# Optimization experiments

Measured on AMD Instinct MI355X. Metric: run time of the kernel, lower is better.

Reference implementation:

```python
import jax, jax.numpy as jnp
import numpy as np

NX, NQ, NU, NY = 256, 64, 8, 4
N = 65536
EPS = 0.01
STD = 0.5


def setup_inputs() -> dict:
    key = jax.random.key(0)
    ks = jax.random.split(key, 8)
    return {
        "x": jax.random.normal(ks[0], (N, NX), jnp.float32),
        "u": jax.random.normal(ks[1], (N, NU), jnp.float32),
        "X": jax.random.normal(ks[2], (NX + NQ, NX + NQ), jnp.float32) * STD,
        "U": jax.random.normal(ks[3], (NX, NQ), jnp.float32) * STD,
        "Y1": jax.random.normal(ks[4], (NX, NX), jnp.float32) * STD,
        "XP": jax.random.normal(ks[5], (NX, NX), jnp.float32) * STD,
        "B2": jax.random.normal(ks[6], (NX, NU), jnp.float32) * STD,
        "D12": jax.random.normal(ks[7], (NQ, NU), jnp.float32) * STD,
        "bv": jnp.zeros((NQ,), jnp.float32),
        "t": 0,
    }


def _constrained(X, U, Y1, XP):
    # updateParameters(): build A, B1, C1, D11 from unconstrained params.
    P = XP @ XP.T + EPS * jnp.eye(NX, dtype=XP.dtype)
    H = X @ X.T + EPS * jnp.eye(NX + NQ, dtype=X.dtype)
    H11, H12, H22 = H[:NX, :NX], H[:NX, NX:], H[NX:, NX:]
    Y = -0.5 * (H11 + Y1 - Y1.T)
    Pinv = jnp.linalg.inv(P)
    A = Pinv @ Y                                   # [nx, nx]
    lam = 0.5 * jnp.diagonal(H22)                  # Lambda diagonal
    D11 = -jnp.tril(H22, -1) / lam[:, None]        # strictly lower triangular [nq, nq]
    C1 = U.T / lam[:, None]                        # [nq, nx]
    B1 = Pinv @ (-H12 - U)                         # [nx, nq]
    return A, B1, C1, D11


def _calc_w(base, D11):
    # Forward substitution: w_i = relu(base_i + sum_{j<i} D11[i,j] * w_j).
    # D11 is strictly lower triangular and unfilled w columns are zero, so a
    # full matvec against the carry is exact.
    nq = base.shape[1]

    def step(w, inp):
        i, row, b_col = inp                        # row: [nq], b_col: [Nbatch]
        wi = jax.nn.relu(b_col + w @ row)
        return w.at[:, i].set(wi), None

    w0 = jnp.zeros_like(base)
    w, _ = jax.lax.scan(step, w0, (jnp.arange(nq), D11, base.T))
    return w


def reference(x, u, X, U, Y1, XP, B2, D12, bv, t):
    A, B1, C1, D11 = _constrained(X, U, Y1, XP)
    base = x @ C1.T + u @ D12.T + bv               # [N, nq]
    w = _calc_w(base, D11)
    x_dot = x @ A.T + w @ B1.T + u @ B2.T          # [N, nx]
    return x_dot
```

## Files before the change

### kernel.cpp

```cpp
#include <hip/hip_runtime.h>

#define EPS_C 0.01f

typedef __attribute__((ext_vector_type(8))) short short8;
typedef __attribute__((ext_vector_type(4))) float f32x4;
typedef __attribute__((ext_vector_type(4))) unsigned short u16x4;
typedef __attribute__((ext_vector_type(8))) unsigned short u16x8;

#define WS_H    0
#define WS_C    102400
#define WS_C2   167936
#define WS_Y    233472
#define WS_RHS  299008
#define WS_D11  331776
#define WS_WFH  419840
#define WS_WFM  464896
#define WS_WFL  509952
#define WS_BBH  555008
#define WS_BBM  564224
#define WS_BBL  573440
#define WS_WG   582656
#define WS_E0   4776960
#define WS_E1   4781056

__device__ __forceinline__ int wfoff(int n, int k) {
    return (((n >> 4) * 44 + (k >> 5) * 4 + ((k >> 3) & 3)) << 7) + ((n & 15) << 3) + (k & 7);
}
__device__ __forceinline__ int bboff(int n, int k) {
    return (((n >> 4) * 36 + (k >> 5) * 4 + ((k >> 3) & 3)) << 7) + ((n & 15) << 3) + (k & 7);
}

__device__ __forceinline__ unsigned short f2bf(float f) {
    unsigned int u = __float_as_uint(f);
    unsigned int r = (u + 0x7fffu + ((u >> 16) & 1u)) >> 16;
    return (unsigned short)r;
}
__device__ __forceinline__ float bf2f(unsigned short h) {
    return __uint_as_float(((unsigned int)h) << 16);
}
__device__ __forceinline__ void split1(float f, unsigned short& h, unsigned short& m, unsigned short& l) {
    h = f2bf(f);
    float r1 = f - bf2f(h);
    m = f2bf(r1);
    l = f2bf(r1 - bf2f(m));
}
__device__ __forceinline__ void split8(const float* v, short8& h8, short8& m8, short8& l8) {
#pragma unroll
    for (int j = 0; j < 8; ++j) {
        unsigned short h, m, l;
        split1(v[j], h, m, l);
        h8[j] = (short)h; m8[j] = (short)m; l8[j] = (short)l;
    }
}

__global__ void k_build(const float* __restrict__ Xm, const float* __restrict__ XPm,
                        float* __restrict__ H, float* __restrict__ P) {
    int idx = blockIdx.x * 256 + threadIdx.x;
    if (idx < 102400) {
        int i = idx / 320, j = idx - i * 320;
        const float4* a = (const float4*)(Xm + i * 320);
        const float4* b = (const float4*)(Xm + j * 320);
        float s = 0.f;
        for (int k = 0; k < 80; ++k) {
            float4 va = a[k], vb = b[k];
            s += va.x * vb.x + va.y * vb.y + va.z * vb.z + va.w * vb.w;
        }
        H[idx] = (i == j) ? s + EPS_C : s;
    } else {
        idx -= 102400;
        if (idx < 65536) {
            int i = idx >> 8, j = idx & 255;
            const float4* a = (const float4*)(XPm + i * 256);
            const float4* b = (const float4*)(XPm + j * 256);
            float s = 0.f;
            for (int k = 0; k < 64; ++k) {
                float4 va = a[k], vb = b[k];
                s += va.x * vb.x + va.y * vb.y + va.z * vb.z + va.w * vb.w;
            }
            P[idx] = (i == j) ? s + EPS_C : s;
        }
    }
}

__global__ void __launch_bounds__(256) k_derived(const float* __restrict__ H, const float* __restrict__ Um,
                          const float* __restrict__ Y1, const float* __restrict__ B2,
                          const float* __restrict__ D12,
                          float* __restrict__ Y, float* __restrict__ RHS,
                          float* __restrict__ D11g,
                          unsigned short* __restrict__ Bh, unsigned short* __restrict__ Bm,
                          unsigned short* __restrict__ Bl,
                          unsigned short* __restrict__ Bbh, unsigned short* __restrict__ Bbm,
                          unsigned short* __restrict__ Bbl,
                          const float* __restrict__ C0, float* __restrict__ E0) {
    __shared__ __align__(16) float M[64 * 68];
    __shared__ __align__(16) float Rs[8 * 68];
    __shared__ __align__(16) float Ts[64 * 8];
    __shared__ float E8s[8 * 9];
    const int tid = threadIdx.x;
    if (blockIdx.x == 441) {
        const int ti = tid & 15, tj = tid >> 4;
#pragma unroll
        for (int t = 0; t < 4; ++t) {
            int e = tid + t * 256;
            int r = e >> 4, c4 = e & 15;
            float4 v = *(const float4*)&C0[(size_t)r * 256 + c4 * 4];
            *(float4*)&M[r * 68 + c4 * 4] = v;
        }
        __syncthreads();
        for (int s = 0; s < 8; ++s) {
            if (tid < 64) {
                const int lane = tid;
                float e8[8];
#pragma unroll
                for (int j = 0; j < 8; ++j) e8[j] = 0.f;
                if (lane < 8) {
#pragma unroll
                    for (int j = 0; j < 8; ++j) e8[j] = M[(s * 8 + lane) * 68 + s * 8 + j];
                }
#pragma unroll
                for (int k = 0; k < 8; ++k) {
                    const float p = __shfl(e8[k], k);
                    const float rinv = 1.0f / p;
                    const float f = -e8[k] * rinv;
                    const bool isk = (lane == k);
#pragma unroll
                    for (int j = 0; j < 8; ++j) {
                        const float prj = __shfl(e8[j], k);
                        if (j == k) e8[j] = isk ? rinv : f;
                        else        e8[j] = isk ? prj * rinv : fmaf(f, prj, e8[j]);
                    }
                }
                if (lane < 8) {
#pragma unroll
                    for (int j = 0; j < 8; ++j) E8s[lane * 9 + j] = e8[j];
                }
            }
            __syncthreads();
#pragma unroll
            for (int t = 0; t < 2; ++t) {
                int e = tid + t * 256;
                int r = e >> 6, c = e & 63;
                Rs[r * 68 + c] = M[(s * 8 + r) * 68 + c];
            }
#pragma unroll
            for (int t = 0; t < 2; ++t) {
                int e = tid + t * 256;
                int i = e >> 3, c = e & 7;
                float acc = 0.f;
#pragma unroll
                for (int j = 0; j < 8; ++j) acc = fmaf(M[i * 68 + s * 8 + j], E8s[j * 9 + c], acc);
                Ts[i * 8 + c] = acc;
            }
            __syncthreads();
            {
                const bool rowIn = ((ti >> 1) == s);
                const bool colIn = ((tj >> 1) == s);
                const int i0 = ti * 4, j0 = tj * 4;
                float nv[4][4];
                if (rowIn && colIn) {
#pragma unroll
                    for (int r = 0; r < 4; ++r)
#pragma unroll
                        for (int d = 0; d < 4; ++d)
                            nv[r][d] = E8s[(i0 - s * 8 + r) * 9 + (j0 - s * 8 + d)];
                } else if (rowIn) {
#pragma unroll
                    for (int r = 0; r < 4; ++r)
#pragma unroll
                        for (int d = 0; d < 4; ++d) {
                            float acc = 0.f;
#pragma unroll
                            for (int c = 0; c < 8; ++c)
                                acc = fmaf(E8s[(i0 - s * 8 + r) * 9 + c], Rs[c * 68 + j0 + d], acc);
                            nv[r][d] = acc;
                        }
                } else if (colIn) {
#pragma unroll
                    for (int r = 0; r < 4; ++r)
#pragma unroll
                        for (int d = 0; d < 4; ++d)
                            nv[r][d] = -Ts[(i0 + r) * 8 + (j0 - s * 8 + d)];
                } else {
#pragma unroll
                    for (int r = 0; r < 4; ++r)
#pragma unroll
                        for (int d = 0; d < 4; ++d) {
                            float acc = M[(i0 + r) * 68 + j0 + d];
#pragma unroll
                            for (int c = 0; c < 8; ++c)
                                acc = fmaf(-Ts[(i0 + r) * 8 + c], Rs[c * 68 + j0 + d], acc);
                            nv[r][d] = acc;
                        }
                }
#pragma unroll
                for (int r = 0; r < 4; ++r)
#pragma unroll
                    for (int d = 0; d < 4; ++d) M[(i0 + r) * 68 + j0 + d] = nv[r][d];
            }
            __syncthreads();
        }
#pragma unroll
        for (int t = 0; t < 4; ++t) {
            int e = tid + t * 256;
            int r = e >> 4, c4 = e & 15;
            float4 v = *(const float4*)&M[r * 68 + c4 * 4];
            *(float4*)&E0[(size_t)r * 64 + c4 * 4] = v;
        }
        return;
    }
    int idx = blockIdx.x * 256 + tid;
    if (idx < 65536) {
        int i = idx >> 8, j = idx & 255;
        Y[idx] = -0.5f * (H[i * 320 + j] + Y1[i * 256 + j] - Y1[j * 256 + i]);
        return;
    }
    idx -= 65536;
    if (idx < 16384) {
        RHS[idx] = -H[(idx >> 6) * 320 + 256 + (idx & 63)] - Um[idx];
        return;
    }
    idx -= 16384;
    if (idx < 4096) {
        int q = idx >> 6, j = idx & 63;
        float lam = 0.5f * H[(256 + q) * 320 + 256 + q];
        D11g[idx] = (j < q) ? -H[(256 + q) * 320 + 256 + j] / lam : 0.f;
        return;
    }
    idx -= 4096;
    if (idx < 8192) {
        int o = idx >> 5, cc = idx & 31;
        float f = (cc < 8) ? B2[o * 8 + cc] : 0.f;
        unsigned short h, m, l;
        split1(f, h, m, l);
        int off = wfoff(o, 256 + cc);
        Bh[off] = h; Bm[off] = m; Bl[off] = l;
        return;
    }
    idx -= 8192;
    if (idx < 18432) {
        int q = idx / 288, k = idx - q * 288;
        float f;
        if (k < 256) {
            float lam = 0.5f * H[(256 + q) * 320 + 256 + q];
            f = Um[(size_t)k * 64 + q] / lam;
        } else if (k < 264) f = D12[(size_t)q * 8 + (k - 256)];
        else f = 0.f;
        unsigned short h, m, l;
        split1(f, h, m, l);
        int off = bboff(q, k);
        Bbh[off] = h; Bbm[off] = m; Bbl[off] = l;
    }
}

__global__ void __launch_bounds__(256) k_gjS(const float* __restrict__ Cold, float* __restrict__ Cnew,
                                             const float* __restrict__ E, float* __restrict__ Eout,
                                             int b, int nb) {
    const int I = blockIdx.x >> 2, J = blockIdx.x & 3;
    const int tid = threadIdx.x;
    const int ti = tid & 15, tj = tid >> 4;
    if (I == b && J == b) {
        const int r = tid >> 2, seg = tid & 3;
#pragma unroll
        for (int t = 0; t < 4; ++t) {
            float4 v = *(const float4*)&E[(size_t)r * 64 + seg * 16 + t * 4];
            *(float4*)&Cnew[(size_t)(b * 64 + r) * 256 + b * 64 + seg * 16 + t * 4] = v;
        }
        return;
    }
    __shared__ __align__(16) float Es[64 * 68];
    __shared__ __align__(16) float S1[64 * 68];
    __shared__ __align__(16) float S2[64 * 68];
    for (int e = tid; e < 1024; e += 256) {
        int r = e >> 4, c4 = e & 15;
        float4 v = *(const float4*)&E[(size_t)r * 64 + c4 * 4];
        *(float4*)&Es[r * 68 + c4 * 4] = v;
    }
    if (I == b) {
        for (int e = tid; e < 1024; e += 256) {
            int r = e >> 4, c4 = e & 15;
            float4 v = *(const float4*)&Cold[(size_t)(b * 64 + r) * 256 + J * 64 + c4 * 4];
            *(float4*)&S1[r * 68 + c4 * 4] = v;
        }
        __syncthreads();
        float acc[4][4];
#pragma unroll
        for (int r = 0; r < 4; ++r)
#pragma unroll
            for (int d = 0; d < 4; ++d) acc[r][d] = 0.f;
        for (int mm = 0; mm < 64; ++mm) {
            float a4[4], b4[4];
#pragma unroll
            for (int d = 0; d < 4; ++d) { a4[d] = Es[(ti * 4 + d) * 68 + mm]; b4[d] = S1[mm * 68 + tj * 4 + d]; }
#pragma unroll
            for (int r = 0; r < 4; ++r)
#pragma unroll
                for (int d = 0; d < 4; ++d) acc[r][d] = fmaf(a4[r], b4[d], acc[r][d]);
        }
#pragma unroll
        for (int r = 0; r < 4; ++r) {
            float4 v = {acc[r][0], acc[r][1], acc[r][2], acc[r][3]};
            *(float4*)&Cnew[(size_t)(b * 64 + ti * 4 + r) * 256 + J * 64 + tj * 4] = v;
        }
        return;
    }
    if (J == b) {
        for (int e = tid; e < 1024; e += 256) {
            int r = e >> 4, c4 = e & 15;
            float4 v = *(const float4*)&Cold[(size_t)(I * 64 + r) * 256 + b * 64 + c4 * 4];
            *(float4*)&S1[r * 68 + c4 * 4] = v;
        }
        __syncthreads();
        float acc[4][4];
#pragma unroll
        for (int r = 0; r < 4; ++r)
#pragma unroll
            for (int d = 0; d < 4; ++d) acc[r][d] = 0.f;
        for (int kk = 0; kk < 64; ++kk) {
            float a4[4], b4[4];
#pragma unroll
            for (int d = 0; d < 4; ++d) { a4[d] = S1[(ti * 4 + d) * 68 + kk]; b4[d] = Es[kk * 68 + tj * 4 + d]; }
#pragma unroll
            for (int r = 0; r < 4; ++r)
#pragma unroll
                for (int d = 0; d < 4; ++d) acc[r][d] = fmaf(a4[r], b4[d], acc[r][d]);
        }
#pragma unroll
        for (int r = 0; r < 4; ++r) {
            float4 v = {-acc[r][0], -acc[r][1], -acc[r][2], -acc[r][3]};
            *(float4*)&Cnew[(size_t)(I * 64 + ti * 4 + r) * 256 + b * 64 + tj * 4] = v;
        }
        return;
    }
    for (int e = tid; e < 1024; e += 256) {
        int r = e >> 4, c4 = e & 15;
        float4 v = *(const float4*)&Cold[(size_t)(I * 64 + r) * 256 + b * 64 + c4 * 4];
        *(float4*)&S1[r * 68 + c4 * 4] = v;
        float4 w = *(const float4*)&Cold[(size_t)(b * 64 + r) * 256 + J * 64 + c4 * 4];
        *(float4*)&S2[r * 68 + c4 * 4] = w;
    }
    __syncthreads();
    float t4[4][4];
#pragma unroll
    for (int r = 0; r < 4; ++r)
#pragma unroll
        for (int d = 0; d < 4; ++d) t4[r][d] = 0.f;
    for (int kk = 0; kk < 64; ++kk) {
        float a4[4], b4[4];
#pragma unroll
        for (int d = 0; d < 4; ++d) { a4[d] = S1[(ti * 4 + d) * 68 + kk]; b4[d] = Es[kk * 68 + tj * 4 + d]; }
#pragma unroll
        for (int r = 0; r < 4; ++r)
#pragma unroll
            for (int d = 0; d < 4; ++d) t4[r][d] = fmaf(a4[r], b4[d], t4[r][d]);
    }
    __syncthreads();
#pragma unroll
    for (int r = 0; r < 4; ++r)
#pragma unroll
        for (int d = 0; d < 4; ++d) S1[(ti * 4 + r) * 68 + tj * 4 + d] = t4[r][d];
    __syncthreads();
    float acc[4][4];
#pragma unroll
    for (int r = 0; r < 4; ++r) {
        float4 cv = *(const float4*)&Cold[(size_t)(I * 64 + ti * 4 + r) * 256 + J * 64 + tj * 4];
        acc[r][0] = cv.x; acc[r][1] = cv.y; acc[r][2] = cv.z; acc[r][3] = cv.w;
    }
    for (int kk = 0; kk < 64; ++kk) {
        float a4[4], b4[4];
#pragma unroll
        for (int d = 0; d < 4; ++d) { a4[d] = S1[(ti * 4 + d) * 68 + kk]; b4[d] = S2[kk * 68 + tj * 4 + d]; }
#pragma unroll
        for (int r = 0; r < 4; ++r)
#pragma unroll
            for (int d = 0; d < 4; ++d) acc[r][d] = fmaf(-a4[r], b4[d], acc[r][d]);
    }
#pragma unroll
    for (int r = 0; r < 4; ++r) {
        float4 v = {acc[r][0], acc[r][1], acc[r][2], acc[r][3]};
        *(float4*)&Cnew[(size_t)(I * 64 + ti * 4 + r) * 256 + J * 64 + tj * 4] = v;
    }
    if (I == nb && J == nb) {
        float* M   = Es;
        float* Rs2 = S2;
        float* Ts2 = S2 + 1024;
        float* E8s = S2 + 1664;
        __syncthreads();
#pragma unroll
        for (int r = 0; r < 4; ++r)
#pragma unroll
            for (int d = 0; d < 4; ++d)
                M[(ti * 4 + r) * 68 + tj * 4 + d] = acc[r][d];
        __syncthreads();
        for (int s = 0; s < 8; ++s) {
            if (tid < 64) {
                const int lane = tid;
                float e8[8];
#pragma unroll
                for (int j = 0; j < 8; ++j) e8[j] = 0.f;
                if (lane < 8) {
#pragma unroll
                    for (int j = 0; j < 8; ++j) e8[j] = M[(s * 8 + lane) * 68 + s * 8 + j];
                }
#pragma unroll
                for (int k = 0; k < 8; ++k) {
                    const float p = __shfl(e8[k], k);
                    const float rinv = 1.0f / p;
                    const float f = -e8[k] * rinv;
                    const bool isk = (lane == k);
#pragma unroll
                    for (int j = 0; j < 8; ++j) {
                        const float prj = __shfl(e8[j], k);
                        if (j == k) e8[j] = isk ? rinv : f;
                        else        e8[j] = isk ? prj * rinv : fmaf(f, prj, e8[j]);
                    }
                }
                if (lane < 8) {
#pragma unroll
                    for (int j = 0; j < 8; ++j) E8s[lane * 9 + j] = e8[j];
                }
            }
            __syncthreads();
#pragma unroll
            for (int t = 0; t < 2; ++t) {
                int e = tid + t * 256;
                int r = e >> 6, c = e & 63;
                Rs2[r * 68 + c] = M[(s * 8 + r) * 68 + c];
            }
#pragma unroll
            for (int t = 0; t < 2; ++t) {
                int e = tid + t * 256;
                int i = e >> 3, c = e & 7;
                float a2 = 0.f;
#pragma unroll
                for (int j = 0; j < 8; ++j) a2 = fmaf(M[i * 68 + s * 8 + j], E8s[j * 9 + c], a2);
                Ts2[i * 8 + c] = a2;
            }
            __syncthreads();
            {
                const bool rowIn = ((ti >> 1) == s);
                const bool colIn = ((tj >> 1) == s);
                const int i0 = ti * 4, j0 = tj * 4;
                float nv[4][4];
                if (rowIn && colIn) {
#pragma unroll
                    for (int r = 0; r < 4; ++r)
#pragma unroll
                        for (int d = 0; d < 4; ++d)
                            nv[r][d] = E8s[(i0 - s * 8 + r) * 9 + (j0 - s * 8 + d)];
                } else if (rowIn) {
#pragma unroll
                    for (int r = 0; r < 4; ++r)
#pragma unroll
                        for (int d = 0; d < 4; ++d) {
                            float a2 = 0.f;
#pragma unroll
                            for (int c = 0; c < 8; ++c)
                                a2 = fmaf(E8s[(i0 - s * 8 + r) * 9 + c], Rs2[c * 68 + j0 + d], a2);
                            nv[r][d] = a2;
                        }
                } else if (colIn) {
#pragma unroll
                    for (int r = 0; r < 4; ++r)
#pragma unroll
                        for (int d = 0; d < 4; ++d)
                            nv[r][d] = -Ts2[(i0 + r) * 8 + (j0 - s * 8 + d)];
                } else {
#pragma unroll
                    for (int r = 0; r < 4; ++r)
#pragma unroll
                        for (int d = 0; d < 4; ++d) {
                            float a2 = M[(i0 + r) * 68 + j0 + d];
#pragma unroll
                            for (int c = 0; c < 8; ++c)
                                a2 = fmaf(-Ts2[(i0 + r) * 8 + c], Rs2[c * 68 + j0 + d], a2);
                            nv[r][d] = a2;
                        }
                }
#pragma unroll
                for (int r = 0; r < 4; ++r)
#pragma unroll
                    for (int d = 0; d < 4; ++d) M[(i0 + r) * 68 + j0 + d] = nv[r][d];
            }
            __syncthreads();
        }
#pragma unroll
        for (int t = 0; t < 4; ++t) {
            int e = tid + t * 256;
            int r = e >> 4, c4 = e & 15;
            float4 v = *(const float4*)&M[r * 68 + c4 * 4];
            *(float4*)&Eout[(size_t)r * 64 + c4 * 4] = v;
        }
    }
}

__global__ void __launch_bounds__(256) k_apply2(const float* __restrict__ PI, const float* __restrict__ Y,
                                                const float* __restrict__ RHS,
                                                unsigned short* __restrict__ Bh, unsigned short* __restrict__ Bm,
                                                unsigned short* __restrict__ Bl) {
    const int i0 = ((int)blockIdx.x / 5) * 64;
    const int c0 = ((int)blockIdx.x % 5) * 64;
    __shared__ __align__(16) float S1[64 * 68], S2[64 * 68];
    const int tid = threadIdx.x;
    const int ti = tid & 15, tj = tid >> 4;
    float acc[4][4];
#pragma unroll
    for (int r = 0; r < 4; ++r)
#pragma unroll
        for (int d = 0; d < 4; ++d) acc[r][d] = 0.f;
    for (int kc = 0; kc < 4; ++kc) {
        __syncthreads();
        for (int e = tid; e < 1024; e += 256) {
            int i = e >> 4, k4 = e & 15;
            float4 v = *(const float4*)&PI[(size_t)(i0 + i) * 256 + kc * 64 + k4 * 4];
            S1[(k4 * 4 + 0) * 68 + i] = v.x;
            S1[(k4 * 4 + 1) * 68 + i] = v.y;
            S1[(k4 * 4 + 2) * 68 + i] = v.z;
            S1[(k4 * 4 + 3) * 68 + i] = v.w;
            float4 w;
            if (c0 < 256) w = *(const float4*)&Y[(size_t)(kc * 64 + i) * 256 + c0 + k4 * 4];
            else          w = *(const float4*)&RHS[(size_t)(kc * 64 + i) * 64 + k4 * 4];
            *(float4*)&S2[i * 68 + k4 * 4] = w;
        }
        __syncthreads();
        for (int kk = 0; kk < 64; ++kk) {
            float4 pv = *(const float4*)&S1[kk * 68 + ti * 4];
            float4 gv = *(const float4*)&S2[kk * 68 + tj * 4];
            float p4[4] = {pv.x, pv.y, pv.z, pv.w};
            float g4[4] = {gv.x, gv.y, gv.z, gv.w};
#pragma unroll
            for (int r = 0; r < 4; ++r)
#pragma unroll
                for (int d = 0; d < 4; ++d) acc[r][d] = fmaf(p4[r], g4[d], acc[r][d]);
        }
    }
    const int pc0 = (c0 < 256) ? c0 : 288;
#pragma unroll
    for (int r = 0; r < 4; ++r)
#pragma unroll
        for (int d = 0; d < 4; ++d) {
            unsigned short h, m, l;
            split1(acc[r][d], h, m, l);
            int off = wfoff(i0 + ti * 4 + r, pc0 + tj * 4 + d);
            Bh[off] = h; Bm[off] = m; Bl[off] = l;
        }
}

#define XSTR 264
__global__ void __launch_bounds__(256, 3) k_base(const float* __restrict__ x, const float* __restrict__ u,
                                                 const unsigned short* __restrict__ Bbh,
                                                 const unsigned short* __restrict__ Bbm,
                                                 const unsigned short* __restrict__ Bbl,
                                                 const float* __restrict__ bv,
                                                 float* __restrict__ wg) {
    __shared__ __align__(16) unsigned short Ah[32 * XSTR];
    __shared__ __align__(16) unsigned short Am[32 * XSTR];
    __shared__ __align__(16) unsigned short Al[32 * XSTR];
    const int tid = threadIdx.x;
    const int r0 = blockIdx.x * 32;
    {
        const float4* xg4 = (const float4*)(x + (size_t)r0 * 256);
#pragma unroll
        for (int i = 0; i < 8; ++i) {
            int e = tid + i * 256, r = e >> 6, c4 = e & 63;
            float4 v = xg4[e];
            float vv[4] = {v.x, v.y, v.z, v.w};
            u16x4 hv, mv, lv;
#pragma unroll
            for (int j = 0; j < 4; ++j) {
                unsigned short h, m, l;
                split1(vv[j], h, m, l);
                hv[j] = h; mv[j] = m; lv[j] = l;
            }
            *(u16x4*)&Ah[r * XSTR + c4 * 4] = hv;
            *(u16x4*)&Am[r * XSTR + c4 * 4] = mv;
            *(u16x4*)&Al[r * XSTR + c4 * 4] = lv;
        }
    }
    __syncthreads();
    const int lane = tid & 63, wid = tid >> 6;
    const int n0 = wid * 16;
    const int lr = lane & 15, lg = lane >> 4;
    const int lk = lg * 8;
    const int fb = wid * 4608 + lg * 128 + lr * 8;
    f32x4 acc[2];
    acc[0] = (f32x4){0.f, 0.f, 0.f, 0.f};
    acc[1] = (f32x4){0.f, 0.f, 0.f, 0.f};
    for (int kt = 0; kt < 9; ++kt) {
        const int ka = kt * 32 + lk;
        short8 a_h[2], a_m[2], a_l[2];
        if (kt < 8) {
            a_h[0] = *(const short8*)&Ah[lr * XSTR + ka];
            a_h[1] = *(const short8*)&Ah[(16 + lr) * XSTR + ka];
            a_m[0] = *(const short8*)&Am[lr * XSTR + ka];
            a_m[1] = *(const short8*)&Am[(16 + lr) * XSTR + ka];
            a_l[0] = *(const short8*)&Al[lr * XSTR + ka];
            a_l[1] = *(const short8*)&Al[(16 + lr) * XSTR + ka];
        } else {
            if (lg == 0) {
                float vv[8];
                const float4* up = (const float4*)&u[(size_t)(r0 + lr) * 8];
                float4 v0 = up[0], v1 = up[1];
                vv[0] = v0.x; vv[1] = v0.y; vv[2] = v0.z; vv[3] = v0.w;
                vv[4] = v1.x; vv[5] = v1.y; vv[6] = v1.z; vv[7] = v1.w;
                split8(vv, a_h[0], a_m[0], a_l[0]);
                const float4* up2 = (const float4*)&u[(size_t)(r0 + 16 + lr) * 8];
                float4 w0 = up2[0], w1 = up2[1];
                vv[0] = w0.x; vv[1] = w0.y; vv[2] = w0.z; vv[3] = w0.w;
                vv[4] = w1.x; vv[5] = w1.y; vv[6] = w1.z; vv[7] = w1.w;
                split8(vv, a_h[1], a_m[1], a_l[1]);
            } else {
                short8 z = {0, 0, 0, 0, 0, 0, 0, 0};
                a_h[0] = z; a_h[1] = z; a_m[0] = z; a_m[1] = z; a_l[0] = z; a_l[1] = z;
            }
        }
        const int off = fb + kt * 512;
        short8 b_h = *(const short8*)&Bbh[off];
        short8 b_m = *(const short8*)&Bbm[off];
        short8 b_l = *(const short8*)&Bbl[off];
#pragma unroll
        for (int m = 0; m < 2; ++m) {
            acc[m] = __builtin_amdgcn_mfma_f32_16x16x32_bf16(a_h[m], b_h, acc[m], 0, 0, 0);
            acc[m] = __builtin_amdgcn_mfma_f32_16x16x32_bf16(a_m[m], b_h, acc[m], 0, 0, 0);
            acc[m] = __builtin_amdgcn_mfma_f32_16x16x32_bf16(a_h[m], b_m, acc[m], 0, 0, 0);
            acc[m] = __builtin_amdgcn_mfma_f32_16x16x32_bf16(a_l[m], b_h, acc[m], 0, 0, 0);
            acc[m] = __builtin_amdgcn_mfma_f32_16x16x32_bf16(a_m[m], b_m, acc[m], 0, 0, 0);
            acc[m] = __builtin_amdgcn_mfma_f32_16x16x32_bf16(a_h[m], b_l, acc[m], 0, 0, 0);
        }
    }
    const float bvv = bv[n0 + lr];
#pragma unroll
    for (int m = 0; m < 2; ++m)
#pragma unroll
        for (int j = 0; j < 4; ++j)
            wg[(size_t)(r0 + m * 16 + lg * 4 + j) * 64 + n0 + lr] = acc[m][j] + bvv;
}

__global__ void __launch_bounds__(256) k_rec(float* __restrict__ wg, const float* __restrict__ D11g) {
    __shared__ float D[64 * 64];
    const int tid = threadIdx.x;
#pragma unroll
    for (int t = 0; t < 16; ++t) D[tid + t * 256] = D11g[tid + t * 256];
    __syncthreads();
    const size_t r = (size_t)blockIdx.x * 256 + tid;
    float w[64];
    float* wr = wg + r * 64;
#pragma unroll
    for (int c = 0; c < 16; ++c) {
        float4 v = *(const float4*)&wr[c * 4];
        w[4 * c] = v.x; w[4 * c + 1] = v.y; w[4 * c + 2] = v.z; w[4 * c + 3] = v.w;
    }
    w[0] = fmaxf(w[0], 0.f);
#pragma unroll
    for (int i = 1; i < 64; ++i) {
        float s0 = w[i], s1 = 0.f, s2 = 0.f, s3 = 0.f;
#pragma unroll
        for (int j = 0; j + 3 < i; j += 4) {
            s0 = fmaf(w[j + 0], D[i * 64 + j + 0], s0);
            s1 = fmaf(w[j + 1], D[i * 64 + j + 1], s1);
            s2 = fmaf(w[j + 2], D[i * 64 + j + 2], s2);
            s3 = fmaf(w[j + 3], D[i * 64 + j + 3], s3);
        }
#pragma unroll
        for (int j = i & ~3; j < i; ++j) s0 = fmaf(w[j], D[i * 64 + j], s0);
        w[i] = fmaxf((s0 + s1) + (s2 + s3), 0.f);
    }
#pragma unroll
    for (int c = 0; c < 16; ++c) {
        float4 v = {w[4 * c], w[4 * c + 1], w[4 * c + 2], w[4 * c + 3]};
        *(float4*)&wr[c * 4] = v;
    }
}

__global__ void __launch_bounds__(256, 3) k_m2(const float* __restrict__ x, const float* __restrict__ wg,
                                               const float* __restrict__ u,
                                               const unsigned short* __restrict__ Bh,
                                               const unsigned short* __restrict__ Bm,
                                               const unsigned short* __restrict__ Bl,
                                               float* __restrict__ out) {
    __shared__ __align__(16) unsigned short Ah[32 * XSTR];
    __shared__ __align__(16) unsigned short Am[32 * XSTR];
    __shared__ __align__(16) unsigned short Al[32 * XSTR];
    const int tid = threadIdx.x;
    const int r0 = blockIdx.x * 32;
    {
        const float4* xg4 = (const float4*)(x + (size_t)r0 * 256);
#pragma unroll
        for (int i = 0; i < 8; ++i) {
            int e = tid + i * 256, r = e >> 6, c4 = e & 63;
            float4 v = xg4[e];
            float vv[4] = {v.x, v.y, v.z, v.w};
            u16x4 hv, mv, lv;
#pragma unroll
            for (int j = 0; j < 4; ++j) {
                unsigned short h, m, l;
                split1(vv[j], h, m, l);
                hv[j] = h; mv[j] = m; lv[j] = l;
            }
            *(u16x4*)&Ah[r * XSTR + c4 * 4] = hv;
            *(u16x4*)&Am[r * XSTR + c4 * 4] = mv;
            *(u16x4*)&Al[r * XSTR + c4 * 4] = lv;
        }
    }
    __syncthreads();
    const int lane = tid & 63, wid = tid >> 6;
    const int n0 = wid * 64;
    const int lr = lane & 15, lg = lane >> 4;
    const int lk = lg * 8;
    const int lgoff = lg * 128 + lr * 8;
    int fb[4];
#pragma unroll
    for (int nf = 0; nf < 4; ++nf) fb[nf] = (wid * 4 + nf) * 5632 + lgoff;
    f32x4 acc[2][4];
#pragma unroll
    for (int m = 0; m < 2; ++m)
#pragma unroll
        for (int nf = 0; nf < 4; ++nf) acc[m][nf] = (f32x4){0.f, 0.f, 0.f, 0.f};

#define M2_MFMA6()                                                                               \
    for (int nf = 0; nf < 4; ++nf) {                                                             \
        for (int m = 0; m < 2; ++m) {                                                            \
            acc[m][nf] = __builtin_amdgcn_mfma_f32_16x16x32_bf16(a_h[m], b_h[nf], acc[m][nf], 0, 0, 0); \
            acc[m][nf] = __builtin_amdgcn_mfma_f32_16x16x32_bf16(a_m[m], b_h[nf], acc[m][nf], 0, 0, 0); \
// ... 55 lines not shown
    }
    for (int kt = 9; kt < 11; ++kt) {
        const int wc = (kt - 9) * 32 + lk;
        short8 a_h[2], a_m[2], a_l[2];
        {
            float vv[8];
            const float4* wp = (const float4*)&wg[(size_t)(r0 + lr) * 64 + wc];
            float4 v0 = wp[0], v1 = wp[1];
            vv[0] = v0.x; vv[1] = v0.y; vv[2] = v0.z; vv[3] = v0.w;
            vv[4] = v1.x; vv[5] = v1.y; vv[6] = v1.z; vv[7] = v1.w;
            split8(vv, a_h[0], a_m[0], a_l[0]);
            const float4* wp2 = (const float4*)&wg[(size_t)(r0 + 16 + lr) * 64 + wc];
            float4 w0 = wp2[0], w1 = wp2[1];
            vv[0] = w0.x; vv[1] = w0.y; vv[2] = w0.z; vv[3] = w0.w;
            vv[4] = w1.x; vv[5] = w1.y; vv[6] = w1.z; vv[7] = w1.w;
            split8(vv, a_h[1], a_m[1], a_l[1]);
        }
        short8 b_h[4], b_m[4], b_l[4];
#pragma unroll
        for (int nf = 0; nf < 4; ++nf) {
            const int off = fb[nf] + kt * 512;
            b_h[nf] = *(const short8*)&Bh[off];
            b_m[nf] = *(const short8*)&Bm[off];
            b_l[nf] = *(const short8*)&Bl[off];
        }
#pragma unroll
        for (int nf = 0; nf < 4; ++nf) {
#pragma unroll
            for (int m = 0; m < 2; ++m) {
                acc[m][nf] = __builtin_amdgcn_mfma_f32_16x16x32_bf16(a_h[m], b_h[nf], acc[m][nf], 0, 0, 0);
                acc[m][nf] = __builtin_amdgcn_mfma_f32_16x16x32_bf16(a_m[m], b_h[nf], acc[m][nf], 0, 0, 0);
                acc[m][nf] = __builtin_amdgcn_mfma_f32_16x16x32_bf16(a_h[m], b_m[nf], acc[m][nf], 0, 0, 0);
                acc[m][nf] = __builtin_amdgcn_mfma_f32_16x16x32_bf16(a_l[m], b_h[nf], acc[m][nf], 0, 0, 0);
                acc[m][nf] = __builtin_amdgcn_mfma_f32_16x16x32_bf16(a_m[m], b_m[nf], acc[m][nf], 0, 0, 0);
                acc[m][nf] = __builtin_amdgcn_mfma_f32_16x16x32_bf16(a_h[m], b_l[nf], acc[m][nf], 0, 0, 0);
                acc[m][nf] = __builtin_amdgcn_mfma_f32_16x16x32_bf16(a_m[m], b_l[nf], acc[m][nf], 0, 0, 0);
                acc[m][nf] = __builtin_amdgcn_mfma_f32_16x16x32_bf16(a_l[m], b_m[nf], acc[m][nf], 0, 0, 0);
            }
        }
    }
#pragma unroll
    for (int m = 0; m < 2; ++m)
#pragma unroll
        for (int nf = 0; nf < 4; ++nf)
#pragma unroll
            for (int j = 0; j < 4; ++j)
                out[(size_t)(r0 + m * 16 + lg * 4 + j) * 256 + n0 + nf * 16 + lr] = acc[m][nf][j];
}

extern "C" void kernel_launch(void* const* d_in, const int* in_sizes, int n_in,
                              void* d_out, int out_size, void* d_ws, size_t ws_size,
                              hipStream_t stream) {
    const float* x   = (const float*)d_in[0];
    const float* u   = (const float*)d_in[1];
    const float* Xm  = (const float*)d_in[2];
    const float* Um  = (const float*)d_in[3];
    const float* Y1  = (const float*)d_in[4];
    const float* XPm = (const float*)d_in[5];
    const float* B2  = (const float*)d_in[6];
    const float* D12 = (const float*)d_in[7];
    const float* bv  = (const float*)d_in[8];
    float* out = (float*)d_out;
    float* ws  = (float*)d_ws;

    float* H    = ws + WS_H;
    float* C0   = ws + WS_C;
    float* C1   = ws + WS_C2;
    float* Y    = ws + WS_Y;
    float* RHS  = ws + WS_RHS;
    float* D11g = ws + WS_D11;
    float* E0   = ws + WS_E0;
    float* E1   = ws + WS_E1;
    unsigned short* Bh  = (unsigned short*)(ws + WS_WFH);
    unsigned short* Bm  = (unsigned short*)(ws + WS_WFM);
    unsigned short* Bl  = (unsigned short*)(ws + WS_WFL);
    unsigned short* Bbh = (unsigned short*)(ws + WS_BBH);
    unsigned short* Bbm = (unsigned short*)(ws + WS_BBM);
    unsigned short* Bbl = (unsigned short*)(ws + WS_BBL);
    float* wg = ws + WS_WG;

    k_build<<<656, 256, 0, stream>>>(Xm, XPm, H, C0);
    k_derived<<<442, 256, 0, stream>>>(H, Um, Y1, B2, D12, Y, RHS, D11g,
                                       Bh, Bm, Bl, Bbh, Bbm, Bbl, C0, E0);
    k_base<<<2048, 256, 0, stream>>>(x, u, Bbh, Bbm, Bbl, bv, wg);
    k_rec<<<256, 256, 0, stream>>>(wg, D11g);
    k_gjS<<<16, 256, 0, stream>>>(C0, C1, E0, E1, 0, 1);
    k_gjS<<<16, 256, 0, stream>>>(C1, C0, E1, E0, 1, 2);
    k_gjS<<<16, 256, 0, stream>>>(C0, C1, E0, E1, 2, 3);
    k_gjS<<<16, 256, 0, stream>>>(C1, C0, E1, E0, 3, -1);
    k_apply2<<<20, 256, 0, stream>>>(C0, Y, RHS, Bh, Bm, Bl);
    k_m2<<<2048, 256, 0, stream>>>(x, wg, u, Bh, Bm, Bl, out);
}
```

Before: 338.0 us.

## Fold first two Gauss-Jordan sweeps into k_base and k_rec as extra blocks

The first two block Gauss-Jordan sweeps of the P inversion are merged into the k_base and k_rec launches as 16 extra blocks each, run on otherwise idle CUs. The intent is to remove two small serial kernel launches and overlap the inversion chain with the batch work. The sweep and 64x64 inversion code is factored into shared device functions. In exchange, k_base and k_rec now reserve a larger shared-memory array sized for the sweep, which may lower their occupancy.

```diff
diff --git a/kernel.cpp b/kernel.cpp
--- a/kernel.cpp
+++ b/kernel.cpp
@@ -78,6 +78,252 @@
                 s += va.x * vb.x + va.y * vb.y + va.z * vb.z + va.w * vb.w;
             }
             P[idx] = (i == j) ? s + EPS_C : s;
+        }
+    }
+}
+
+__device__ __forceinline__ void inv64_lds(float* M, float* Rs, float* Ts, float* E8s,
+                                          int tid, int ti, int tj) {
+    for (int s = 0; s < 8; ++s) {
+        if (tid < 64) {
+            const int lane = tid;
+            float e8[8];
+#pragma unroll
+            for (int j = 0; j < 8; ++j) e8[j] = 0.f;
+            if (lane < 8) {
+#pragma unroll
+                for (int j = 0; j < 8; ++j) e8[j] = M[(s * 8 + lane) * 68 + s * 8 + j];
+            }
+#pragma unroll
+            for (int k = 0; k < 8; ++k) {
+                const float p = __shfl(e8[k], k);
+                const float rinv = 1.0f / p;
+                const float f = -e8[k] * rinv;
+                const bool isk = (lane == k);
+#pragma unroll
+                for (int j = 0; j < 8; ++j) {
+                    const float prj = __shfl(e8[j], k);
+                    if (j == k) e8[j] = isk ? rinv : f;
+                    else        e8[j] = isk ? prj * rinv : fmaf(f, prj, e8[j]);
+                }
+            }
+            if (lane < 8) {
+#pragma unroll
+                for (int j = 0; j < 8; ++j) E8s[lane * 9 + j] = e8[j];
+            }
+        }
+        __syncthreads();
+#pragma unroll
+        for (int t = 0; t < 2; ++t) {
+            int e = tid + t * 256;
+            int r = e >> 6, c = e & 63;
+            Rs[r * 68 + c] = M[(s * 8 + r) * 68 + c];
+        }
+#pragma unroll
+        for (int t = 0; t < 2; ++t) {
+            int e = tid + t * 256;
+            int i = e >> 3, c = e & 7;
+            float acc = 0.f;
+#pragma unroll
+            for (int j = 0; j < 8; ++j) acc = fmaf(M[i * 68 + s * 8 + j], E8s[j * 9 + c], acc);
+            Ts[i * 8 + c] = acc;
+        }
+        __syncthreads();
+        {
+            const bool rowIn = ((ti >> 1) == s);
+            const bool colIn = ((tj >> 1) == s);
+            const int i0 = ti * 4, j0 = tj * 4;
+            float nv[4][4];
+            if (rowIn && colIn) {
+#pragma unroll
+                for (int r = 0; r < 4; ++r)
+#pragma unroll
+                    for (int d = 0; d < 4; ++d)
+                        nv[r][d] = E8s[(i0 - s * 8 + r) * 9 + (j0 - s * 8 + d)];
+            } else if (rowIn) {
+#pragma unroll
+                for (int r = 0; r < 4; ++r)
+#pragma unroll
+                    for (int d = 0; d < 4; ++d) {
+                        float acc = 0.f;
+#pragma unroll
+                        for (int c = 0; c < 8; ++c)
+                            acc = fmaf(E8s[(i0 - s * 8 + r) * 9 + c], Rs[c * 68 + j0 + d], acc);
+                        nv[r][d] = acc;
+                    }
+            } else if (colIn) {
+#pragma unroll
+                for (int r = 0; r < 4; ++r)
+#pragma unroll
+                    for (int d = 0; d < 4; ++d)
+                        nv[r][d] = -Ts[(i0 + r) * 8 + (j0 - s * 8 + d)];
+            } else {
+#pragma unroll
+                for (int r = 0; r < 4; ++r)
+#pragma unroll
+                    for (int d = 0; d < 4; ++d) {
+                        float acc = M[(i0 + r) * 68 + j0 + d];
+#pragma unroll
+                        for (int c = 0; c < 8; ++c)
+                            acc = fmaf(-Ts[(i0 + r) * 8 + c], Rs[c * 68 + j0 + d], acc);
+                        nv[r][d] = acc;
+                    }
+            }
+#pragma unroll
+            for (int r = 0; r < 4; ++r)
+#pragma unroll
+                for (int d = 0; d < 4; ++d) M[(i0 + r) * 68 + j0 + d] = nv[r][d];
+        }
+        __syncthreads();
+    }
+}
+
+__device__ void gj_sweep(float* SM, const float* __restrict__ Cold, float* __restrict__ Cnew,
+                         const float* __restrict__ E, float* __restrict__ Eout,
+                         int b, int nb, int bid) {
+    float* Es = SM;
+    float* S1 = SM + 4352;
+    float* S2 = SM + 8704;
+    const int tid = threadIdx.x;
+    const int I = bid >> 2, J = bid & 3;
+    const int ti = tid & 15, tj = tid >> 4;
+    if (I == b && J == b) {
+        const int r = tid >> 2, seg = tid & 3;
+#pragma unroll
+        for (int t = 0; t < 4; ++t) {
+            float4 v = *(const float4*)&E[(size_t)r * 64 + seg * 16 + t * 4];
+            *(float4*)&Cnew[(size_t)(b * 64 + r) * 256 + b * 64 + seg * 16 + t * 4] = v;
+        }
+        return;
+    }
+    for (int e = tid; e < 1024; e += 256) {
+        int r = e >> 4, c4 = e & 15;
+        float4 v = *(const float4*)&E[(size_t)r * 64 + c4 * 4];
+        *(float4*)&Es[r * 68 + c4 * 4] = v;
+    }
+    if (I == b) {
+        for (int e = tid; e < 1024; e += 256) {
+            int r = e >> 4, c4 = e & 15;
+            float4 v = *(const float4*)&Cold[(size_t)(b * 64 + r) * 256 + J * 64 + c4 * 4];
+            *(float4*)&S1[r * 68 + c4 * 4] = v;
+        }
+        __syncthreads();
+        float acc[4][4];
+#pragma unroll
+        for (int r = 0; r < 4; ++r)
+#pragma unroll
+            for (int d = 0; d < 4; ++d) acc[r][d] = 0.f;
+        for (int mm = 0; mm < 64; ++mm) {
+            float a4[4], b4[4];
+#pragma unroll
+            for (int d = 0; d < 4; ++d) { a4[d] = Es[(ti * 4 + d) * 68 + mm]; b4[d] = S1[mm * 68 + tj * 4 + d]; }
+#pragma unroll
+            for (int r = 0; r < 4; ++r)
+#pragma unroll
+                for (int d = 0; d < 4; ++d) acc[r][d] = fmaf(a4[r], b4[d], acc[r][d]);
+        }
+#pragma unroll
+        for (int r = 0; r < 4; ++r) {
+            float4 v = {acc[r][0], acc[r][1], acc[r][2], acc[r][3]};
+            *(float4*)&Cnew[(size_t)(b * 64 + ti * 4 + r) * 256 + J * 64 + tj * 4] = v;
+        }
+        return;
+    }
+    if (J == b) {
+        for (int e = tid; e < 1024; e += 256) {
+            int r = e >> 4, c4 = e & 15;
+            float4 v = *(const float4*)&Cold[(size_t)(I * 64 + r) * 256 + b * 64 + c4 * 4];
+            *(float4*)&S1[r * 68 + c4 * 4] = v;
+        }
+        __syncthreads();
+        float acc[4][4];
+#pragma unroll
+        for (int r = 0; r < 4; ++r)
+#pragma unroll
+            for (int d = 0; d < 4; ++d) acc[r][d] = 0.f;
+        for (int kk = 0; kk < 64; ++kk) {
+            float a4[4], b4[4];
+#pragma unroll
+            for (int d = 0; d < 4; ++d) { a4[d] = S1[(ti * 4 + d) * 68 + kk]; b4[d] = Es[kk * 68 + tj * 4 + d]; }
+#pragma unroll
+            for (int r = 0; r < 4; ++r)
+#pragma unroll
+                for (int d = 0; d < 4; ++d) acc[r][d] = fmaf(a4[r], b4[d], acc[r][d]);
+        }
+#pragma unroll
+        for (int r = 0; r < 4; ++r) {
+            float4 v = {-acc[r][0], -acc[r][1], -acc[r][2], -acc[r][3]};
+            *(float4*)&Cnew[(size_t)(I * 64 + ti * 4 + r) * 256 + b * 64 + tj * 4] = v;
+        }
+        return;
+    }
+    for (int e = tid; e < 1024; e += 256) {
+        int r = e >> 4, c4 = e & 15;
+        float4 v = *(const float4*)&Cold[(size_t)(I * 64 + r) * 256 + b * 64 + c4 * 4];
+        *(float4*)&S1[r * 68 + c4 * 4] = v;
+        float4 w = *(const float4*)&Cold[(size_t)(b * 64 + r) * 256 + J * 64 + c4 * 4];
+        *(float4*)&S2[r * 68 + c4 * 4] = w;
+    }
+    __syncthreads();
+    float t4[4][4];
+#pragma unroll
+    for (int r = 0; r < 4; ++r)
+#pragma unroll
+        for (int d = 0; d < 4; ++d) t4[r][d] = 0.f;
+    for (int kk = 0; kk < 64; ++kk) {
+        float a4[4], b4[4];
+#pragma unroll
+        for (int d = 0; d < 4; ++d) { a4[d] = S1[(ti * 4 + d) * 68 + kk]; b4[d] = Es[kk * 68 + tj * 4 + d]; }
+#pragma unroll
+        for (int r = 0; r < 4; ++r)
+#pragma unroll
+            for (int d = 0; d < 4; ++d) t4[r][d] = fmaf(a4[r], b4[d], t4[r][d]);
+    }
+    __syncthreads();
+#pragma unroll
+    for (int r = 0; r < 4; ++r)
+#pragma unroll
+        for (int d = 0; d < 4; ++d) S1[(ti * 4 + r) * 68 + tj * 4 + d] = t4[r][d];
+    __syncthreads();
+    float acc[4][4];
+#pragma unroll
+    for (int r = 0; r < 4; ++r) {
+        float4 cv = *(const float4*)&Cold[(size_t)(I * 64 + ti * 4 + r) * 256 + J * 64 + tj * 4];
+        acc[r][0] = cv.x; acc[r][1] = cv.y; acc[r][2] = cv.z; acc[r][3] = cv.w;
+    }
+    for (int kk = 0; kk < 64; ++kk) {
+        float a4[4], b4[4];
+#pragma unroll
+        for (int d = 0; d < 4; ++d) { a4[d] = S1[(ti * 4 + d) * 68 + kk]; b4[d] = S2[kk * 68 + tj * 4 + d]; }
+#pragma unroll
+        for (int r = 0; r < 4; ++r)
+#pragma unroll
+            for (int d = 0; d < 4; ++d) acc[r][d] = fmaf(-a4[r], b4[d], acc[r][d]);
+    }
+#pragma unroll
+    for (int r = 0; r < 4; ++r) {
+        float4 v = {acc[r][0], acc[r][1], acc[r][2], acc[r][3]};
+        *(float4*)&Cnew[(size_t)(I * 64 + ti * 4 + r) * 256 + J * 64 + tj * 4] = v;
+    }
+    if (I == nb && J == nb) {
+        float* M   = Es;
+        float* Rs2 = S2;
+        float* Ts2 = S2 + 1024;
+        float* E8s = S2 + 1664;
+        __syncthreads();
+#pragma unroll
+        for (int r = 0; r < 4; ++r)
+#pragma unroll
+            for (int d = 0; d < 4; ++d)
+                M[(ti * 4 + r) * 68 + tj * 4 + d] = acc[r][d];
+        __syncthreads();
+        inv64_lds(M, Rs2, Ts2, E8s, tid, ti, tj);
+#pragma unroll
+        for (int t = 0; t < 4; ++t) {
+            int e = tid + t * 256;
+            int r = e >> 4, c4 = e & 15;
+            float4 v = *(const float4*)&M[r * 68 + c4 * 4];
+            *(float4*)&Eout[(size_t)r * 64 + c4 * 4] = v;
         }
     }
 }
@@ -107,98 +353,7 @@
             *(float4*)&M[r * 68 + c4 * 4] = v;
         }
         __syncthreads();
-        for (int s = 0; s < 8; ++s) {
-            if (tid < 64) {
-                const int lane = tid;
-                float e8[8];
-#pragma unroll
-                for (int j = 0; j < 8; ++j) e8[j] = 0.f;
-                if (lane < 8) {
-#pragma unroll
-                    for (int j = 0; j < 8; ++j) e8[j] = M[(s * 8 + lane) * 68 + s * 8 + j];
-                }
-#pragma unroll
-                for (int k = 0; k < 8; ++k) {
-                    const float p = __shfl(e8[k], k);
-                    const float rinv = 1.0f / p;
-                    const float f = -e8[k] * rinv;
-                    const bool isk = (lane == k);
-#pragma unroll
-                    for (int j = 0; j < 8; ++j) {
-                        const float prj = __shfl(e8[j], k);
-                        if (j == k) e8[j] = isk ? rinv : f;
-                        else        e8[j] = isk ? prj * rinv : fmaf(f, prj, e8[j]);
-                    }
-                }
-                if (lane < 8) {
-#pragma unroll
-                    for (int j = 0; j < 8; ++j) E8s[lane * 9 + j] = e8[j];
-                }
-            }
-            __syncthreads();
-#pragma unroll
-            for (int t = 0; t < 2; ++t) {
-                int e = tid + t * 256;
-                int r = e >> 6, c = e & 63;
-                Rs[r * 68 + c] = M[(s * 8 + r) * 68 + c];
-            }
-#pragma unroll
-            for (int t = 0; t < 2; ++t) {
-                int e = tid + t * 256;
-                int i = e >> 3, c = e & 7;
-                float acc = 0.f;
-#pragma unroll
-                for (int j = 0; j < 8; ++j) acc = fmaf(M[i * 68 + s * 8 + j], E8s[j * 9 + c], acc);
-                Ts[i * 8 + c] = acc;
-            }
-            __syncthreads();
-            {
-                const bool rowIn = ((ti >> 1) == s);
-                const bool colIn = ((tj >> 1) == s);
-                const int i0 = ti * 4, j0 = tj * 4;
-                float nv[4][4];
-                if (rowIn && colIn) {
-#pragma unroll
-                    for (int r = 0; r < 4; ++r)
-#pragma unroll
-                        for (int d = 0; d < 4; ++d)
-                            nv[r][d] = E8s[(i0 - s * 8 + r) * 9 + (j0 - s * 8 + d)];
-                } else if (rowIn) {
-#pragma unroll
-                    for (int r = 0; r < 4; ++r)
-#pragma unroll
-                        for (int d = 0; d < 4; ++d) {
-                            float acc = 0.f;
-#pragma unroll
-                            for (int c = 0; c < 8; ++c)
-                                acc = fmaf(E8s[(i0 - s * 8 + r) * 9 + c], Rs[c * 68 + j0 + d], acc);
-                            nv[r][d] = acc;
-                        }
-                } else if (colIn) {
-#pragma unroll
-                    for (int r = 0; r < 4; ++r)
-#pragma unroll
-                        for (int d = 0; d < 4; ++d)
-                            nv[r][d] = -Ts[(i0 + r) * 8 + (j0 - s * 8 + d)];
-                } else {
-#pragma unroll
-                    for (int r = 0; r < 4; ++r)
-#pragma unroll
-                        for (int d = 0; d < 4; ++d) {
-                            float acc = M[(i0 + r) * 68 + j0 + d];
-#pragma unroll
-                            for (int c = 0; c < 8; ++c)
-                                acc = fmaf(-Ts[(i0 + r) * 8 + c], Rs[c * 68 + j0 + d], acc);
-                            nv[r][d] = acc;
-                        }
-                }
-#pragma unroll
-                for (int r = 0; r < 4; ++r)
-#pragma unroll
-                    for (int d = 0; d < 4; ++d) M[(i0 + r) * 68 + j0 + d] = nv[r][d];
-            }
-            __syncthreads();
-        }
+        inv64_lds(M, Rs, Ts, E8s, tid, ti, tj);
 #pragma unroll
         for (int t = 0; t < 4; ++t) {
             int e = tid + t * 256;
@@ -255,242 +410,8 @@
 __global__ void __launch_bounds__(256) k_gjS(const float* __restrict__ Cold, float* __restrict__ Cnew,
                                              const float* __restrict__ E, float* __restrict__ Eout,
                                              int b, int nb) {
-    const int I = blockIdx.x >> 2, J = blockIdx.x & 3;
-    const int tid = threadIdx.x;
-    const int ti = tid & 15, tj = tid >> 4;
-    if (I == b && J == b) {
-        const int r = tid >> 2, seg = tid & 3;
-#pragma unroll
-        for (int t = 0; t < 4; ++t) {
-            float4 v = *(const float4*)&E[(size_t)r * 64 + seg * 16 + t * 4];
-            *(float4*)&Cnew[(size_t)(b * 64 + r) * 256 + b * 64 + seg * 16 + t * 4] = v;
-        }
-        return;
-    }
-    __shared__ __align__(16) float Es[64 * 68];
-    __shared__ __align__(16) float S1[64 * 68];
-    __shared__ __align__(16) float S2[64 * 68];
-    for (int e = tid; e < 1024; e += 256) {
-        int r = e >> 4, c4 = e & 15;
-        float4 v = *(const float4*)&E[(size_t)r * 64 + c4 * 4];
-        *(float4*)&Es[r * 68 + c4 * 4] = v;
-    }
-    if (I == b) {
-        for (int e = tid; e < 1024; e += 256) {
-            int r = e >> 4, c4 = e & 15;
-            float4 v = *(const float4*)&Cold[(size_t)(b * 64 + r) * 256 + J * 64 + c4 * 4];
-            *(float4*)&S1[r * 68 + c4 * 4] = v;
-        }
-        __syncthreads();
-        float acc[4][4];
-#pragma unroll
-        for (int r = 0; r < 4; ++r)
-#pragma unroll
-            for (int d = 0; d < 4; ++d) acc[r][d] = 0.f;
-        for (int mm = 0; mm < 64; ++mm) {
-            float a4[4], b4[4];
-#pragma unroll
-            for (int d = 0; d < 4; ++d) { a4[d] = Es[(ti * 4 + d) * 68 + mm]; b4[d] = S1[mm * 68 + tj * 4 + d]; }
-#pragma unroll
-            for (int r = 0; r < 4; ++r)
-#pragma unroll
-                for (int d = 0; d < 4; ++d) acc[r][d] = fmaf(a4[r], b4[d], acc[r][d]);
-        }
-#pragma unroll
-        for (int r = 0; r < 4; ++r) {
-            float4 v = {acc[r][0], acc[r][1], acc[r][2], acc[r][3]};
-            *(float4*)&Cnew[(size_t)(b * 64 + ti * 4 + r) * 256 + J * 64 + tj * 4] = v;
-        }
-        return;
-    }
-    if (J == b) {
-        for (int e = tid; e < 1024; e += 256) {
-            int r = e >> 4, c4 = e & 15;
-            float4 v = *(const float4*)&Cold[(size_t)(I * 64 + r) * 256 + b * 64 + c4 * 4];
-            *(float4*)&S1[r * 68 + c4 * 4] = v;
-        }
-        __syncthreads();
-        float acc[4][4];
-#pragma unroll
-        for (int r = 0; r < 4; ++r)
-#pragma unroll
-            for (int d = 0; d < 4; ++d) acc[r][d] = 0.f;
-        for (int kk = 0; kk < 64; ++kk) {
-            float a4[4], b4[4];
-#pragma unroll
-            for (int d = 0; d < 4; ++d) { a4[d] = S1[(ti * 4 + d) * 68 + kk]; b4[d] = Es[kk * 68 + tj * 4 + d]; }
-#pragma unroll
-            for (int r = 0; r < 4; ++r)
-#pragma unroll
-                for (int d = 0; d < 4; ++d) acc[r][d] = fmaf(a4[r], b4[d], acc[r][d]);
-        }
-#pragma unroll
-        for (int r = 0; r < 4; ++r) {
-            float4 v = {-acc[r][0], -acc[r][1], -acc[r][2], -acc[r][3]};
-            *(float4*)&Cnew[(size_t)(I * 64 + ti * 4 + r) * 256 + b * 64 + tj * 4] = v;
-        }
-        return;
-    }
-    for (int e = tid; e < 1024; e += 256) {
-        int r = e >> 4, c4 = e & 15;
-        float4 v = *(const float4*)&Cold[(size_t)(I * 64 + r) * 256 + b * 64 + c4 * 4];
-        *(float4*)&S1[r * 68 + c4 * 4] = v;
-        float4 w = *(const float4*)&Cold[(size_t)(b * 64 + r) * 256 + J * 64 + c4 * 4];
-        *(float4*)&S2[r * 68 + c4 * 4] = w;
-    }
-    __syncthreads();
-    float t4[4][4];
-#pragma unroll
-    for (int r = 0; r < 4; ++r)
-#pragma unroll
-        for (int d = 0; d < 4; ++d) t4[r][d] = 0.f;
-    for (int kk = 0; kk < 64; ++kk) {
-        float a4[4], b4[4];
-#pragma unroll
-        for (int d = 0; d < 4; ++d) { a4[d] = S1[(ti * 4 + d) * 68 + kk]; b4[d] = Es[kk * 68 + tj * 4 + d]; }
-#pragma unroll
-        for (int r = 0; r < 4; ++r)
-#pragma unroll
-            for (int d = 0; d < 4; ++d) t4[r][d] = fmaf(a4[r], b4[d], t4[r][d]);
-    }
-    __syncthreads();
-#pragma unroll
-    for (int r = 0; r < 4; ++r)
-#pragma unroll
-        for (int d = 0; d < 4; ++d) S1[(ti * 4 + r) * 68 + tj * 4 + d] = t4[r][d];
-    __syncthreads();
-    float acc[4][4];
-#pragma unroll
-    for (int r = 0; r < 4; ++r) {
-        float4 cv = *(const float4*)&Cold[(size_t)(I * 64 + ti * 4 + r) * 256 + J * 64 + tj * 4];
-        acc[r][0] = cv.x; acc[r][1] = cv.y; acc[r][2] = cv.z; acc[r][3] = cv.w;
-    }
-    for (int kk = 0; kk < 64; ++kk) {
-        float a4[4], b4[4];
-#pragma unroll
-        for (int d = 0; d < 4; ++d) { a4[d] = S1[(ti * 4 + d) * 68 + kk]; b4[d] = S2[kk * 68 + tj * 4 + d]; }
-#pragma unroll
-        for (int r = 0; r < 4; ++r)
-#pragma unroll
-            for (int d = 0; d < 4; ++d) acc[r][d] = fmaf(-a4[r], b4[d], acc[r][d]);
-    }
-#pragma unroll
-    for (int r = 0; r < 4; ++r) {
-        float4 v = {acc[r][0], acc[r][1], acc[r][2], acc[r][3]};
-        *(float4*)&Cnew[(size_t)(I * 64 + ti * 4 + r) * 256 + J * 64 + tj * 4] = v;
-    }
-    if (I == nb && J == nb) {
-        float* M   = Es;
-        float* Rs2 = S2;
-        float* Ts2 = S2 + 1024;
-        float* E8s = S2 + 1664;
-        __syncthreads();
-#pragma unroll
-        for (int r = 0; r < 4; ++r)
-#pragma unroll
-            for (int d = 0; d < 4; ++d)
-                M[(ti * 4 + r) * 68 + tj * 4 + d] = acc[r][d];
-        __syncthreads();
-        for (int s = 0; s < 8; ++s) {
-            if (tid < 64) {
-                const int lane = tid;
-                float e8[8];
-#pragma unroll
-                for (int j = 0; j < 8; ++j) e8[j] = 0.f;
-                if (lane < 8) {
-#pragma unroll
-                    for (int j = 0; j < 8; ++j) e8[j] = M[(s * 8 + lane) * 68 + s * 8 + j];
-                }
-#pragma unroll
-                for (int k = 0; k < 8; ++k) {
-                    const float p = __shfl(e8[k], k);
-                    const float rinv = 1.0f / p;
-                    const float f = -e8[k] * rinv;
-                    const bool isk = (lane == k);
-#pragma unroll
-                    for (int j = 0; j < 8; ++j) {
-                        const float prj = __shfl(e8[j], k);
-                        if (j == k) e8[j] = isk ? rinv : f;
-                        else        e8[j] = isk ? prj * rinv : fmaf(f, prj, e8[j]);
-                    }
-                }
-                if (lane < 8) {
-#pragma unroll
-                    for (int j = 0; j < 8; ++j) E8s[lane * 9 + j] = e8[j];
-                }
-            }
-            __syncthreads();
-#pragma unroll
-            for (int t = 0; t < 2; ++t) {
-                int e = tid + t * 256;
-                int r = e >> 6, c = e & 63;
-                Rs2[r * 68 + c] = M[(s * 8 + r) * 68 + c];
-            }
-#pragma unroll
-            for (int t = 0; t < 2; ++t) {
-                int e = tid + t * 256;
-                int i = e >> 3, c = e & 7;
-                float a2 = 0.f;
-#pragma unroll
-                for (int j = 0; j < 8; ++j) a2 = fmaf(M[i * 68 + s * 8 + j], E8s[j * 9 + c], a2);
-                Ts2[i * 8 + c] = a2;
-            }
-            __syncthreads();
-            {
-                const bool rowIn = ((ti >> 1) == s);
-                const bool colIn = ((tj >> 1) == s);
-                const int i0 = ti * 4, j0 = tj * 4;
-                float nv[4][4];
-                if (rowIn && colIn) {
-#pragma unroll
-                    for (int r = 0; r < 4; ++r)
-#pragma unroll
-                        for (int d = 0; d < 4; ++d)
-                            nv[r][d] = E8s[(i0 - s * 8 + r) * 9 + (j0 - s * 8 + d)];
-                } else if (rowIn) {
-#pragma unroll
-                    for (int r = 0; r < 4; ++r)
-#pragma unroll
-                        for (int d = 0; d < 4; ++d) {
-                            float a2 = 0.f;
-#pragma unroll
-                            for (int c = 0; c < 8; ++c)
-                                a2 = fmaf(E8s[(i0 - s * 8 + r) * 9 + c], Rs2[c * 68 + j0 + d], a2);
-                            nv[r][d] = a2;
-                        }
-                } else if (colIn) {
-#pragma unroll
-                    for (int r = 0; r < 4; ++r)
-#pragma unroll
-                        for (int d = 0; d < 4; ++d)
-                            nv[r][d] = -Ts2[(i0 + r) * 8 + (j0 - s * 8 + d)];
-                } else {
-#pragma unroll
-                    for (int r = 0; r < 4; ++r)
-#pragma unroll
-                        for (int d = 0; d < 4; ++d) {
-                            float a2 = M[(i0 + r) * 68 + j0 + d];
-#pragma unroll
-                            for (int c = 0; c < 8; ++c)
-                                a2 = fmaf(-Ts2[(i0 + r) * 8 + c], Rs2[c * 68 + j0 + d], a2);
-                            nv[r][d] = a2;
-                        }
-                }
-#pragma unroll
-                for (int r = 0; r < 4; ++r)
-#pragma unroll
-                    for (int d = 0; d < 4; ++d) M[(i0 + r) * 68 + j0 + d] = nv[r][d];
-            }
-            __syncthreads();
-        }
-#pragma unroll
-        for (int t = 0; t < 4; ++t) {
-            int e = tid + t * 256;
-            int r = e >> 4, c4 = e & 15;
-            float4 v = *(const float4*)&M[r * 68 + c4 * 4];
-            *(float4*)&Eout[(size_t)r * 64 + c4 * 4] = v;
-        }
-    }
+    __shared__ __align__(16) float SM[13056];
+    gj_sweep(SM, Cold, Cnew, E, Eout, b, nb, blockIdx.x);
 }
 
 __global__ void __launch_bounds__(256) k_apply2(const float* __restrict__ PI, const float* __restrict__ Y,
@@ -551,11 +472,18 @@
                                                  const unsigned short* __restrict__ Bbm,
                                                  const unsigned short* __restrict__ Bbl,
                                                  const float* __restrict__ bv,
-                                                 float* __restrict__ wg) {
-    __shared__ __align__(16) unsigned short Ah[32 * XSTR];
-    __shared__ __align__(16) unsigned short Am[32 * XSTR];
-    __shared__ __align__(16) unsigned short Al[32 * XSTR];
+                                                 float* __restrict__ wg,
+                                                 const float* __restrict__ C0, float* __restrict__ C1,
+                                                 const float* __restrict__ E0, float* __restrict__ E1) {
+    __shared__ __align__(16) float SM[13056];
     const int tid = threadIdx.x;
+    if (blockIdx.x >= 2048) {
+        gj_sweep(SM, C0, C1, E0, E1, 0, 1, blockIdx.x - 2048);
+        return;
+    }
+    unsigned short* Ah = (unsigned short*)SM;
+    unsigned short* Am = Ah + 32 * XSTR;
+    unsigned short* Al = Am + 32 * XSTR;
     const int r0 = blockIdx.x * 32;
     {
         const float4* xg4 = (const float4*)(x + (size_t)r0 * 256);
@@ -635,9 +563,16 @@
             wg[(size_t)(r0 + m * 16 + lg * 4 + j) * 64 + n0 + lr] = acc[m][j] + bvv;
 }
 
-__global__ void __launch_bounds__(256) k_rec(float* __restrict__ wg, const float* __restrict__ D11g) {
-    __shared__ float D[64 * 64];
+__global__ void __launch_bounds__(256) k_rec(float* __restrict__ wg, const float* __restrict__ D11g,
+                                             const float* __restrict__ C1, float* __restrict__ C0,
+                                             const float* __restrict__ E1, float* __restrict__ E0) {
+    __shared__ __align__(16) float SM[13056];
     const int tid = threadIdx.x;
+    if (blockIdx.x >= 256) {
+        gj_sweep(SM, C1, C0, E1, E0, 1, 2, blockIdx.x - 256);
+        return;
+    }
+    float* D = SM;
 #pragma unroll
     for (int t = 0; t < 16; ++t) D[tid + t * 256] = D11g[tid + t * 256];
     __syncthreads();
@@ -859,10 +794,8 @@
     k_build<<<656, 256, 0, stream>>>(Xm, XPm, H, C0);
     k_derived<<<442, 256, 0, stream>>>(H, Um, Y1, B2, D12, Y, RHS, D11g,
                                        Bh, Bm, Bl, Bbh, Bbm, Bbl, C0, E0);
-    k_base<<<2048, 256, 0, stream>>>(x, u, Bbh, Bbm, Bbl, bv, wg);
-    k_rec<<<256, 256, 0, stream>>>(wg, D11g);
-    k_gjS<<<16, 256, 0, stream>>>(C0, C1, E0, E1, 0, 1);
-    k_gjS<<<16, 256, 0, stream>>>(C1, C0, E1, E0, 1, 2);
+    k_base<<<2064, 256, 0, stream>>>(x, u, Bbh, Bbm, Bbl, bv, wg, C0, C1, E0, E1);
+    k_rec<<<272, 256, 0, stream>>>(wg, D11g, C1, C0, E1, E0);
     k_gjS<<<16, 256, 0, stream>>>(C0, C1, E0, E1, 2, 3);
     k_gjS<<<16, 256, 0, stream>>>(C1, C0, E1, E0, 3, -1);
     k_apply2<<<20, 256, 0, stream>>>(C0, Y, RHS, Bh, Bm, Bl);
```

Result: slower. 415.0 us (+22.8%).
